# Performance work log

Measured on AMD Instinct MI355X. Metric: run time of the kernel, lower is better.

Reference implementation:

```python
import jax, jax.numpy as jnp
import numpy as np

N = 100000   # nodes
E = 1600000  # edges (avg degree 16)
R = 8        # relations
B = 4        # bases
IN = 128     # in_size
H = 128      # hidden_size
OUT = 64     # out_feats


def setup_inputs() -> dict:
    key = jax.random.key(0)
    k = jax.random.split(key, 14)
    sI = 1.0 / np.sqrt(IN)
    sH = 1.0 / np.sqrt(H)
    sB = 1.0 / np.sqrt(B)
    return {
        "feat": jax.random.normal(k[0], (N, IN), jnp.float32),
        "win": jax.random.normal(k[1], (IN, H), jnp.float32) * sI,
        "bin_": jnp.zeros((H,), jnp.float32),
        "basis0": jax.random.normal(k[2], (B, H, H), jnp.float32) * sH,
        "wcomp0": jax.random.normal(k[3], (R, B), jnp.float32) * sB,
        "loop0": jax.random.normal(k[4], (H, H), jnp.float32) * sH,
        "hbias0": jnp.zeros((H,), jnp.float32),
        "basis1": jax.random.normal(k[5], (B, H, H), jnp.float32) * sH,
        "wcomp1": jax.random.normal(k[6], (R, B), jnp.float32) * sB,
        "loop1": jax.random.normal(k[7], (H, H), jnp.float32) * sH,
        "hbias1": jnp.zeros((H,), jnp.float32),
        "wout": jax.random.normal(k[8], (H, OUT), jnp.float32) * sH,
        "bout": jnp.zeros((OUT,), jnp.float32),
        "src": jax.random.randint(k[9], (E,), 0, N),
        "dst": jax.random.randint(k[10], (E,), 0, N),
        "etypes": jax.random.randint(k[11], (E,), 0, R),
    }


def _rel_graph_conv(h, src, dst, etypes, basis, wcomp, loopw, hbias):
    """DGL RelGraphConv (basis regularizer, self_loop, bias, relu).

    out_i = relu( sum_r W_r * (sum_{e: dst_e=i, etype_e=r} h[src_e]) + h_i @ loopw + bias )
    Messages are linear, so we aggregate raw features by (dst, relation)
    composite key first, then apply the R per-relation matmuls once per node.
    """
    W = jnp.einsum('rb,bio->rio', wcomp, basis)          # [R, H, H] basis-composed weights
    seg = dst * R + etypes                               # composite (node, relation) key
    s = jax.ops.segment_sum(h[src], seg, num_segments=N * R)  # [N*R, H]
    s = s.reshape(N, R, -1)
    agg = jnp.einsum('nri,rio->no', s, W)                # [N, H]
    return jax.nn.relu(agg + hbias + h @ loopw)


def reference(feat, win, bin_, basis0, wcomp0, loop0, hbias0,
              basis1, wcomp1, loop1, hbias1, wout, bout, src, dst, etypes):
    h = jax.nn.relu(feat @ win + bin_)                   # input_layer
    h = _rel_graph_conv(h, src, dst, etypes, basis0, wcomp0, loop0, hbias0)
    h = _rel_graph_conv(h, src, dst, etypes, basis1, wcomp1, loop1, hbias1)
    return jax.nn.relu(h @ wout + bout)                  # out_layer
```

## Files before the change

### kernel.cpp

```cpp
#include <hip/hip_runtime.h>

#define NN   100000
#define EE   1600000
constexpr int RR = 8;
constexpr int BBASES = 4;
constexpr int SCAN_CHUNK = 1024;
constexpr int NBLK = (NN + SCAN_CHUNK - 1) / SCAN_CHUNK;
constexpr int NBUK = 98;
constexpr int EPB  = 4096;
constexpr int P1BLOCKS = (EE + EPB - 1) / EPB;

typedef __attribute__((ext_vector_type(8))) short short8;
typedef __attribute__((ext_vector_type(4))) float f32x4;

__device__ __forceinline__ unsigned pack2(float x, float y) {
    unsigned xu = __float_as_uint(x);
    unsigned yu = __float_as_uint(y);
    xu = (xu + 0x7fffu + ((xu >> 16) & 1u)) >> 16;
    yu = (yu + 0x7fffu + ((yu >> 16) & 1u)) & 0xffff0000u;
    return xu | yu;
}

__device__ __forceinline__ unsigned short bf16r(float x) {
    unsigned u = __float_as_uint(x);
    return (unsigned short)((u + 0x7fffu + ((u >> 16) & 1u)) >> 16);
}

__device__ __forceinline__ void async16(const void* g, void* l) {
    __builtin_amdgcn_global_load_lds(
        (const __attribute__((address_space(1))) void*)g,
        (__attribute__((address_space(3))) void*)l, 16, 0, 0);
}


__global__ __launch_bounds__(256) void count_kernel(const int* __restrict__ dst,
                                                    int* __restrict__ counts) {
    int e = blockIdx.x * 256 + threadIdx.x;
    if (e < EE) atomicAdd(&counts[dst[e]], 1);
}

__global__ __launch_bounds__(256) void scan1(const int* __restrict__ counts,
                                             int* __restrict__ offsets,
                                             int* __restrict__ totals) {
    __shared__ int lds[256];
    int b = blockIdx.x, tid = threadIdx.x;
    int base = b * SCAN_CHUNK + tid * 4;
    int v0 = (base + 0 < NN) ? counts[base + 0] : 0;
    int v1 = (base + 1 < NN) ? counts[base + 1] : 0;
    int v2 = (base + 2 < NN) ? counts[base + 2] : 0;
    int v3 = (base + 3 < NN) ? counts[base + 3] : 0;
    int s0 = v0, s1 = s0 + v1, s2 = s1 + v2, s3 = s2 + v3;
    lds[tid] = s3;
    __syncthreads();
    for (int d = 1; d < 256; d <<= 1) {
        int x = (tid >= d) ? lds[tid - d] : 0;
        __syncthreads();
        lds[tid] += x;
        __syncthreads();
    }
    int incl = lds[tid];
    int prefix = incl - s3;
    if (base + 0 < NN) offsets[base + 0] = prefix;
    if (base + 1 < NN) offsets[base + 1] = prefix + s0;
    if (base + 2 < NN) offsets[base + 2] = prefix + s1;
    if (base + 3 < NN) offsets[base + 3] = prefix + s2;
    if (tid == 255) totals[b] = lds[255];
}

__global__ __launch_bounds__(128) void scan2(int* __restrict__ totals,
                                             int* __restrict__ offsets,
                                             int* __restrict__ gcursor) {
    __shared__ int s[128];
    int tid = threadIdx.x;
    int v = (tid < NBLK) ? totals[tid] : 0;
    s[tid] = v;
    __syncthreads();
    for (int d = 1; d < 128; d <<= 1) {
        int x = (tid >= d) ? s[tid - d] : 0;
        __syncthreads();
        s[tid] += x;
        __syncthreads();
    }
    int excl = s[tid] - v;
    if (tid < NBLK) {
        totals[tid] = excl;
        gcursor[tid] = excl;
    }
    if (tid == NBLK - 1) offsets[NN] = excl + v;
}

__global__ __launch_bounds__(256) void scan3(int* __restrict__ offsets,
                                             const int* __restrict__ totals) {
    int i = blockIdx.x * 256 + threadIdx.x;
    if (i < NN) offsets[i] += totals[i >> 10];
}


__global__ __launch_bounds__(256) void bin_pass1(const int* __restrict__ src,
                                                 const int* __restrict__ dst,
                                                 const int* __restrict__ et,
                                                 int* __restrict__ gcursor,
                                                 unsigned* __restrict__ tmp) {
    __shared__ unsigned stage[EPB];
    __shared__ int hist[128];
    __shared__ int sc[128];
    __shared__ int lb[128];
    __shared__ int gb[128];
    int tid = threadIdx.x;
    long e0 = (long)blockIdx.x * EPB;
    if (tid < 128) hist[tid] = 0;
    __syncthreads();

    unsigned w[16];
    int bk[16], pos[16];
#pragma unroll
    for (int i = 0; i < 16; ++i) {
        long e = e0 + i * 256 + tid;
        bool valid = e < EE;
        int d = valid ? dst[e] : 0;
        int s = valid ? src[e] : 0;
        int r = valid ? et[e] : 0;
        bk[i] = d >> 10;
        w[i] = (unsigned)s | ((unsigned)r << 17) | ((unsigned)(d & 1023) << 20);
        pos[i] = valid ? atomicAdd(&hist[bk[i]], 1) : -1;
    }
    __syncthreads();
    if (tid < 128) sc[tid] = hist[tid];
    __syncthreads();
    for (int d = 1; d < 128; d <<= 1) {
        int v = 0;
        if (tid < 128 && tid >= d) v = sc[tid - d];
        __syncthreads();
        if (tid < 128) sc[tid] += v;
        __syncthreads();
    }
    if (tid < 128) lb[tid] = sc[tid] - hist[tid];
    if (tid < NBUK && hist[tid] > 0) gb[tid] = atomicAdd(&gcursor[tid], hist[tid]);
    __syncthreads();
    int total = sc[127];
#pragma unroll
    for (int i = 0; i < 16; ++i) {
        if (pos[i] >= 0) stage[lb[bk[i]] + pos[i]] = w[i];
    }
    __syncthreads();
    for (int s = tid; s < total; s += 256) {
        int lo = 0, hi = 127;
#pragma unroll
        for (int it = 0; it < 7; ++it) {
            int mid = (lo + hi + 1) >> 1;
            if (lb[mid] <= s) lo = mid; else hi = mid - 1;
        }
        tmp[gb[lo] + (s - lb[lo])] = stage[s];
    }
}

__global__ __launch_bounds__(1024) void bin_pass2(const unsigned* __restrict__ tmp,
                                                  const int* __restrict__ offsets,
                                                  int* __restrict__ packed) {
    __shared__ int hist[8192];
    __shared__ int ssum[1024];
    int b = blockIdx.x, tid = threadIdx.x;
    int nb0 = b << 10;
    int nend = nb0 + 1024; if (nend > NN) nend = NN;
    int beg = offsets[nb0], end = offsets[nend];
#pragma unroll
    for (int i = 0; i < 8; ++i) hist[tid * 8 + i] = 0;
    __syncthreads();
    for (int e = beg + tid; e < end; e += 1024) {
        unsigned wv = tmp[e];
        atomicAdd(&hist[(wv >> 17) & 8191], 1);
    }
    __syncthreads();
    int loc[8];
    int run = 0;
#pragma unroll
    for (int i = 0; i < 8; ++i) { loc[i] = run; run += hist[tid * 8 + i]; }
    ssum[tid] = run;
    __syncthreads();
    for (int d = 1; d < 1024; d <<= 1) {
        int x = (tid >= d) ? ssum[tid - d] : 0;
        __syncthreads();
        ssum[tid] += x;
        __syncthreads();
    }
    int base = (tid > 0) ? ssum[tid - 1] : 0;
#pragma unroll
    for (int i = 0; i < 8; ++i) hist[tid * 8 + i] = base + loc[i];
    __syncthreads();
    for (int e = beg + tid; e < end; e += 1024) {
        unsigned wv = tmp[e];
        int p = beg + atomicAdd(&hist[(wv >> 17) & 8191], 1);
        packed[p] = (int)((wv & 0x1FFFFu) | (((wv >> 17) & 7u) << 20));
    }
}


__global__ __launch_bounds__(256) void convert_weights(const float* __restrict__ basis0,
                                                       const float* __restrict__ loop0,
                                                       const float* __restrict__ basis1,
                                                       const float* __restrict__ loop1,
                                                       const float* __restrict__ win,
                                                       const float* __restrict__ wout,
                                                       unsigned short* __restrict__ BT0,
                                                       unsigned short* __restrict__ BT1,
                                                       unsigned short* __restrict__ winT,
                                                       unsigned short* __restrict__ woutT) {
    int i = blockIdx.x * 256 + threadIdx.x;
    if (i < 81920) {
        int n = i / 640, k = i % 640;
        BT0[i] = bf16r(k < 512 ? basis0[(size_t)k * 128 + n] : loop0[(size_t)(k - 512) * 128 + n]);
    } else if (i < 163840) {
        int j = i - 81920;
        int n = j / 640, k = j % 640;
        BT1[j] = bf16r(k < 512 ? basis1[(size_t)k * 128 + n] : loop1[(size_t)(k - 512) * 128 + n]);
    } else if (i < 180224) {
        int j = i - 163840;
        int n = j >> 7, k = j & 127;
        winT[j] = bf16r(win[(size_t)k * 128 + n]);
    } else if (i < 188416) {
        int j = i - 180224;
        int n = j >> 7, k = j & 127;
        woutT[j] = bf16r(wout[(size_t)k * 64 + n]);
    }
}

template <int NC, bool F32OUT, bool AF32>
__global__ __launch_bounds__(256) void gemm128(const void* __restrict__ Aptr,
                                               const unsigned short* __restrict__ BT,
                                               const float* __restrict__ bias,
                                               void* __restrict__ outp, int M) {
    constexpr int NFRAG = NC / 32;
    constexpr int BQ = NC * 8 / 256;
    __shared__ __align__(16) char As[2][16384];
    __shared__ __align__(16) char Bs[2][NC * 128];
    int tid = threadIdx.x;
    int lane = tid & 63;
    int wave = tid >> 6;
    int wm = wave >> 1, wn = wave & 1;
    int m0 = blockIdx.x * 128;

    uint4 areg[4], breg[BQ];
    auto loadA = [&](int c) {
#pragma unroll
        for (int q = 0; q < 4; ++q) {
            int lin = q * 256 + tid;
            int row = lin >> 3, slot = lin & 7;
            int gr = m0 + row;
            gr = (gr < M) ? gr : (M - 1);
            if (AF32) {
                const float* fp = (const float*)Aptr + (size_t)gr * 128 + c * 64 + slot * 8;
                float4 v0 = *(const float4*)fp;
                float4 v1 = *(const float4*)(fp + 4);
                areg[q].x = pack2(v0.x, v0.y);
                areg[q].y = pack2(v0.z, v0.w);
                areg[q].z = pack2(v1.x, v1.y);
                areg[q].w = pack2(v1.z, v1.w);
            } else {
                areg[q] = *(const uint4*)((const char*)Aptr + (size_t)gr * 256 + c * 128 + slot * 16);
            }
        }
    };
    auto loadB = [&](int c) {
#pragma unroll
        for (int q = 0; q < BQ; ++q) {
            int lin = q * 256 + tid;
            int n = lin >> 3, slot = lin & 7;
            breg[q] = *(const uint4*)((const char*)BT + (size_t)n * 256 + c * 128 + slot * 16);
        }
    };

    f32x4 acc[4][NFRAG];
#pragma unroll
    for (int m = 0; m < 4; ++m)
#pragma unroll
        for (int n = 0; n < NFRAG; ++n) acc[m][n] = (f32x4)0.f;

    loadA(0); loadB(0);
    int swz = (lane & 7) << 4;

    for (int c = 0; c < 2; ++c) {
        int buf = c & 1;
#pragma unroll
        for (int q = 0; q < 4; ++q) {
            int lin = q * 256 + tid;
            int row = lin >> 3, slot = lin & 7;
            *(uint4*)(As[buf] + row * 128 + ((slot * 16) ^ ((row & 7) << 4))) = areg[q];
        }
#pragma unroll
        for (int q = 0; q < BQ; ++q) {
            int lin = q * 256 + tid;
            int row = lin >> 3, slot = lin & 7;
            *(uint4*)(Bs[buf] + row * 128 + ((slot * 16) ^ ((row & 7) << 4))) = breg[q];
        }
        __syncthreads();
        if (c < 1) { loadA(1); loadB(1); }
#pragma unroll
        for (int ks = 0; ks < 2; ++ks) {
            short8 a[4], b[NFRAG];
            int kb = ks * 64 + (lane >> 4) * 16;
#pragma unroll
            for (int m = 0; m < 4; ++m) {
                int row = wm * 64 + m * 16 + (lane & 15);
                a[m] = *(const short8*)(As[buf] + row * 128 + (kb ^ swz));
            }
#pragma unroll
            for (int n = 0; n < NFRAG; ++n) {
                int col = wn * (NC / 2) + n * 16 + (lane & 15);
                b[n] = *(const short8*)(Bs[buf] + col * 128 + (kb ^ swz));
            }
#pragma unroll
            for (int m = 0; m < 4; ++m)
#pragma unroll
                for (int n = 0; n < NFRAG; ++n)
                    acc[m][n] = __builtin_amdgcn_mfma_f32_16x16x32_bf16(a[m], b[n], acc[m][n], 0, 0, 0);
        }
        __syncthreads();
    }

    int colbase = wn * (NC / 2) + (lane & 15);
    float bias_v[NFRAG];
#pragma unroll
    for (int n = 0; n < NFRAG; ++n) bias_v[n] = bias[colbase + n * 16];
#pragma unroll
    for (int m = 0; m < 4; ++m) {
        int rl0 = m0 + wm * 64 + m * 16 + ((lane >> 4) << 2);
#pragma unroll
        for (int n = 0; n < NFRAG; ++n) {
            int col = colbase + n * 16;
#pragma unroll
            for (int q = 0; q < 4; ++q) {
                float v = fmaxf(acc[m][n][q] + bias_v[n], 0.f);
                int row = rl0 + q;
                if (F32OUT) {
                    if (row < M) ((float*)outp)[(size_t)row * NC + col] = v;
                } else {
                    float vo = __shfl_xor(v, 1);
                    if (((lane & 1) == 0) && row < M)
                        ((unsigned*)outp)[(size_t)row * (NC / 2) + (col >> 1)] = pack2(v, vo);
                }
            }
        }
    }
}


__global__ __launch_bounds__(256) void agg_kernel(const unsigned* __restrict__ hin,
                                                  const int* __restrict__ offsets,
                                                  const int* __restrict__ packed,
                                                  const float* __restrict__ wcomp,
                                                  unsigned* __restrict__ tbuf,
                                                  int chunk_start, int chunk_len) {
    __shared__ float wc[32];
    int tid = threadIdx.x;
    if (tid < 32) wc[tid] = wcomp[tid];
    __syncthreads();
    int nl = blockIdx.x * 4 + (tid >> 6);
    int lane = tid & 63;
    if (nl >= chunk_len) return;
    int n = chunk_start + nl;
    int beg = offsets[n], end = offsets[n + 1];

    float t0 = 0.f, t1 = 0.f, t2 = 0.f, t3 = 0.f;
    float t4 = 0.f, t5 = 0.f, t6 = 0.f, t7 = 0.f;
    float sx = 0.f, sy = 0.f;
    int rcur = -1;

    auto fold = [&]() {
        float w0 = wc[rcur * 4 + 0], w1 = wc[rcur * 4 + 1];
        float w2 = wc[rcur * 4 + 2], w3 = wc[rcur * 4 + 3];
        t0 = fmaf(w0, sx, t0); t1 = fmaf(w0, sy, t1);
        t2 = fmaf(w1, sx, t2); t3 = fmaf(w1, sy, t3);
        t4 = fmaf(w2, sx, t4); t5 = fmaf(w2, sy, t5);
        t6 = fmaf(w3, sx, t6); t7 = fmaf(w3, sy, t7);
        sx = 0.f; sy = 0.f;
    };
    auto acc1 = [&](unsigned u, unsigned hv) {
        int r = (int)(u >> 20);
        if (r != rcur) {
            if (rcur >= 0) fold();
            rcur = r;
        }
        sx += __uint_as_float(hv << 16);
        sy += __uint_as_float(hv & 0xffff0000u);
    };

    int e = beg;
    int ehead = (beg + 3) & ~3;
    if (ehead > end) ehead = end;
    for (; e < ehead; ++e) {
        unsigned u = (unsigned)packed[e];
        unsigned hv = hin[(size_t)(u & 0xFFFFFu) * 64 + lane];
        acc1(u, hv);
    }
    for (; e + 8 <= end; e += 8) {
        uint4 p0 = *(const uint4*)(packed + e);
        uint4 p1 = *(const uint4*)(packed + e + 4);
        unsigned h0 = hin[(size_t)(p0.x & 0xFFFFFu) * 64 + lane];
        unsigned h1 = hin[(size_t)(p0.y & 0xFFFFFu) * 64 + lane];
        unsigned h2 = hin[(size_t)(p0.z & 0xFFFFFu) * 64 + lane];
        unsigned h3 = hin[(size_t)(p0.w & 0xFFFFFu) * 64 + lane];
        unsigned h4 = hin[(size_t)(p1.x & 0xFFFFFu) * 64 + lane];
        unsigned h5 = hin[(size_t)(p1.y & 0xFFFFFu) * 64 + lane];
        unsigned h6 = hin[(size_t)(p1.z & 0xFFFFFu) * 64 + lane];
        unsigned h7 = hin[(size_t)(p1.w & 0xFFFFFu) * 64 + lane];
        acc1(p0.x, h0); acc1(p0.y, h1); acc1(p0.z, h2); acc1(p0.w, h3);
        acc1(p1.x, h4); acc1(p1.y, h5); acc1(p1.z, h6); acc1(p1.w, h7);
    }
    for (; e + 4 <= end; e += 4) {
        uint4 p0 = *(const uint4*)(packed + e);
        unsigned h0 = hin[(size_t)(p0.x & 0xFFFFFu) * 64 + lane];
        unsigned h1 = hin[(size_t)(p0.y & 0xFFFFFu) * 64 + lane];
        unsigned h2 = hin[(size_t)(p0.z & 0xFFFFFu) * 64 + lane];
        unsigned h3 = hin[(size_t)(p0.w & 0xFFFFFu) * 64 + lane];
        acc1(p0.x, h0); acc1(p0.y, h1); acc1(p0.z, h2); acc1(p0.w, h3);
    }
    for (; e < end; ++e) {
        unsigned u = (unsigned)packed[e];
        unsigned hv = hin[(size_t)(u & 0xFFFFFu) * 64 + lane];
        acc1(u, hv);
    }
    if (rcur >= 0) fold();

    size_t tb = (size_t)nl * 256 + lane;
    __builtin_nontemporal_store(pack2(t0, t1), &tbuf[tb + 0]);
    __builtin_nontemporal_store(pack2(t2, t3), &tbuf[tb + 64]);
    __builtin_nontemporal_store(pack2(t4, t5), &tbuf[tb + 128]);
    __builtin_nontemporal_store(pack2(t6, t7), &tbuf[tb + 192]);
}


template <bool FUSE_OUT>
__global__ __launch_bounds__(256) void conv_gemm(const unsigned* __restrict__ tbuf,
                                                 const unsigned* __restrict__ hin,
                                                 const unsigned short* __restrict__ BT,
                                                 const float* __restrict__ hbias,
                                                 unsigned* __restrict__ hout,
                                                 const unsigned short* __restrict__ WoutT,
                                                 const float* __restrict__ bout,
                                                 float* __restrict__ outp,
                                                 int chunk_start, int chunk_len) {
    __shared__ __align__(16) char As[2][16384];
    __shared__ __align__(16) char Bs[2][16384];
    __shared__ __align__(16) char Ws[16384];
    int tid = threadIdx.x;
    int lane = tid & 63;
    int wave = tid >> 6;
    int wm = wave >> 1, wn = wave & 1;
    int m0 = blockIdx.x * 128;

    auto stage = [&](int c, int buf) {
#pragma unroll
        for (int q = 0; q < 4; ++q) {
            int row = q * 32 + wave * 8 + (lane >> 3);
            int s_src = (lane & 7) ^ (lane >> 3);
            int lr = m0 + row;
            lr = (lr < chunk_len) ? lr : (chunk_len - 1);
            const char* ga = (c < 8)
                ? (const char*)(tbuf + (size_t)lr * 256) + c * 128 + s_src * 16
                : (const char*)(hin + (size_t)(chunk_start + lr) * 64) + (c - 8) * 128 + s_src * 16;
            async16(ga, &As[buf][q * 4096 + wave * 1024]);
            const char* gb = (const char*)BT + (size_t)row * 1280 + c * 128 + s_src * 16;
            async16(gb, &Bs[buf][q * 4096 + wave * 1024]);
        }
    };

    f32x4 acc[4][4];
#pragma unroll
    for (int m = 0; m < 4; ++m)
#pragma unroll
        for (int n = 0; n < 4; ++n) acc[m][n] = (f32x4)0.f;

    stage(0, 0);
    if (FUSE_OUT) {
#pragma unroll
        for (int q = 0; q < 4; ++q) {
            int row = q * 16 + wave * 4 + (lane >> 4);
            int s_src = (lane & 15) ^ (row & 7);
            async16((const char*)WoutT + (size_t)row * 256 + s_src * 16,
                    &Ws[q * 4096 + wave * 1024]);
        }
    }
    __syncthreads();
    int swz = (lane & 7) << 4;

    for (int c = 0; c < 10; ++c) {
        int buf = c & 1;
        if (c < 9) stage(c + 1, buf ^ 1);
#pragma unroll
        for (int ks = 0; ks < 2; ++ks) {
            short8 a[4], b[4];
            int kb = ks * 64 + (lane >> 4) * 16;
#pragma unroll
            for (int m = 0; m < 4; ++m) {
                int row = wm * 64 + m * 16 + (lane & 15);
                a[m] = *(const short8*)(As[buf] + row * 128 + (kb ^ swz));
            }
#pragma unroll
            for (int n = 0; n < 4; ++n) {
                int col = wn * 64 + n * 16 + (lane & 15);
                b[n] = *(const short8*)(Bs[buf] + col * 128 + (kb ^ swz));
            }
#pragma unroll
            for (int m = 0; m < 4; ++m)
#pragma unroll
                for (int n = 0; n < 4; ++n)
                    acc[m][n] = __builtin_amdgcn_mfma_f32_16x16x32_bf16(a[m], b[n], acc[m][n], 0, 0, 0);
        }
        __syncthreads();
    }

    unsigned* olds = (unsigned*)&As[0][0];
    int colbase = wn * 64 + (lane & 15);
    float bias_v[4];
#pragma unroll
    for (int n = 0; n < 4; ++n) bias_v[n] = hbias[colbase + n * 16];

    if (!FUSE_OUT) {
#pragma unroll
        for (int m = 0; m < 4; ++m) {
            int rbase = wm * 64 + m * 16 + ((lane >> 4) << 2);
#pragma unroll
            for (int n = 0; n < 4; ++n) {
#pragma unroll
                for (int q = 0; q < 4; ++q) {
                    float v = fmaxf(acc[m][n][q] + bias_v[n], 0.f);
                    float vo = __shfl_xor(v, 1);
                    if ((lane & 1) == 0) {
                        olds[(rbase + q) * 64 + wn * 32 + n * 8 + ((lane & 15) >> 1)] = pack2(v, vo);
                    }
                }
            }
        }
        __syncthreads();
#pragma unroll
        for (int i = 0; i < 8; ++i) {
            int j = i * 256 + tid;
            int row = j >> 4, s = j & 15;
            int gr = m0 + row;
            if (gr < chunk_len) {
                ((uint4*)(hout + (size_t)(chunk_start + gr) * 64))[s] = ((const uint4*)olds)[j];
            }
        }
    } else {
#pragma unroll
        for (int m = 0; m < 4; ++m) {
            int rbase = wm * 64 + m * 16 + ((lane >> 4) << 2);
#pragma unroll
            for (int n = 0; n < 4; ++n) {
#pragma unroll
                for (int q = 0; q < 4; ++q) {
                    float v = fmaxf(acc[m][n][q] + bias_v[n], 0.f);
                    float vo = __shfl_xor(v, 1);
                    if ((lane & 1) == 0) {
                        int row = rbase + q;
                        int d = wn * 32 + n * 8 + ((lane & 15) >> 1);
                        olds[row * 64 + (d ^ ((row & 7) << 2))] = pack2(v, vo);
                    }
                }
            }
        }
        __syncthreads();
        f32x4 acc2[4][2];
#pragma unroll
        for (int m = 0; m < 4; ++m)
#pragma unroll
            for (int n = 0; n < 2; ++n) acc2[m][n] = (f32x4)0.f;
#pragma unroll
        for (int ks = 0; ks < 4; ++ks) {
            int kb = ks * 64 + (lane >> 4) * 16;
            short8 a2[4], b2[2];
#pragma unroll
            for (int m = 0; m < 4; ++m) {
                int row = wm * 64 + m * 16 + (lane & 15);
                a2[m] = *(const short8*)((const char*)olds + row * 256 + (kb ^ ((row & 7) << 4)));
            }
#pragma unroll
            for (int n = 0; n < 2; ++n) {
                int col = wn * 32 + n * 16 + (lane & 15);
                b2[n] = *(const short8*)(Ws + col * 256 + (kb ^ ((col & 7) << 4)));
            }
#pragma unroll
            for (int m = 0; m < 4; ++m)
#pragma unroll
                for (int n = 0; n < 2; ++n)
                    acc2[m][n] = __builtin_amdgcn_mfma_f32_16x16x32_bf16(a2[m], b2[n], acc2[m][n], 0, 0, 0);
        }
        int colb = wn * 32 + (lane & 15);
        float bv2[2];
#pragma unroll
        for (int n = 0; n < 2; ++n) bv2[n] = bout[colb + n * 16];
#pragma unroll
        for (int m = 0; m < 4; ++m) {
            int rl0 = wm * 64 + m * 16 + ((lane >> 4) << 2);
#pragma unroll
            for (int n = 0; n < 2; ++n) {
#pragma unroll
                for (int q = 0; q < 4; ++q) {
                    int row = rl0 + q;
                    if (m0 + row < chunk_len) {
                        float v = fmaxf(acc2[m][n][q] + bv2[n], 0.f);
                        outp[(size_t)(chunk_start + m0 + row) * 64 + colb + n * 16] = v;
                    }
                }
            }
        }
    }
}


static inline size_t align256(size_t x) { return (x + 255) & ~(size_t)255; }

extern "C" void kernel_launch(void* const* d_in, const int* in_sizes, int n_in,
                              void* d_out, int out_size, void* d_ws, size_t ws_size,
                              hipStream_t stream) {
    const float* feat   = (const float*)d_in[0];
    const float* win    = (const float*)d_in[1];
    const float* bin_   = (const float*)d_in[2];
    const float* basis0 = (const float*)d_in[3];
    const float* wcomp0 = (const float*)d_in[4];
    const float* loop0  = (const float*)d_in[5];
    const float* hbias0 = (const float*)d_in[6];
    const float* basis1 = (const float*)d_in[7];
    const float* wcomp1 = (const float*)d_in[8];
    const float* loop1  = (const float*)d_in[9];
    const float* hbias1 = (const float*)d_in[10];
    const float* wout   = (const float*)d_in[11];
    const float* bout   = (const float*)d_in[12];
    const int*   src    = (const int*)d_in[13];
    const int*   dst    = (const int*)d_in[14];
    const int*   etyp   = (const int*)d_in[15];
    float* outp = (float*)d_out;

    size_t off = 0;
    char* wsb = (char*)d_ws;
    auto walloc = [&](size_t bytes) { void* p = wsb + off; off += align256(bytes); return p; };
    unsigned* hA  = (unsigned*)walloc((size_t)NN * 64 * 4);
    unsigned* hB  = (unsigned*)walloc((size_t)NN * 64 * 4);
    int* offsets  = (int*)walloc((size_t)(NN + 1) * 4);
    int* counts   = (int*)walloc((size_t)NN * 4);
    int* totals   = (int*)walloc((size_t)NBLK * 4);
    int* gcursor  = (int*)walloc((size_t)NBUK * 4);
    int* packed   = (int*)walloc((size_t)EE * 4);
    unsigned* tmp = (unsigned*)walloc((size_t)EE * 4);
    unsigned short* BT0 = (unsigned short*)walloc((size_t)128 * 640 * 2);
    unsigned short* BT1 = (unsigned short*)walloc((size_t)128 * 640 * 2);
    unsigned short* winT = (unsigned short*)walloc((size_t)128 * 128 * 2);
    unsigned short* woutT = (unsigned short*)walloc((size_t)64 * 128 * 2);
    size_t fixed = off;

    int nchunk = 1;
    while (nchunk < 32) {
        size_t rows = (size_t)(NN + nchunk - 1) / nchunk;
        if (fixed + rows * 1024 <= ws_size) break;
        nchunk *= 2;
    }
    int chunk_rows = (NN + nchunk - 1) / nchunk;
    unsigned* tbuf = (unsigned*)(wsb + fixed);

    hipMemsetAsync(counts, 0, (size_t)NN * 4, stream);
    count_kernel<<<(EE + 255) / 256, 256, 0, stream>>>(dst, counts);
    scan1<<<NBLK, 256, 0, stream>>>(counts, offsets, totals);
    scan2<<<1, 128, 0, stream>>>(totals, offsets, gcursor);
    scan3<<<(NN + 255) / 256, 256, 0, stream>>>(offsets, totals);
    bin_pass1<<<P1BLOCKS, 256, 0, stream>>>(src, dst, etyp, gcursor, tmp);
    bin_pass2<<<NBUK, 1024, 0, stream>>>(tmp, offsets, packed);

    convert_weights<<<(188416 + 255) / 256, 256, 0, stream>>>(
        basis0, loop0, basis1, loop1, win, wout, BT0, BT1, winT, woutT);

    int gblocks = (NN + 127) / 128;
    gemm128<128, false, true><<<gblocks, 256, 0, stream>>>(feat, winT, bin_, hA, NN);

    for (int s = 0; s < NN; s += chunk_rows) {
        int len = (NN - s < chunk_rows) ? (NN - s) : chunk_rows;
        agg_kernel<<<(len + 3) / 4, 256, 0, stream>>>(hA, offsets, packed, wcomp0, tbuf, s, len);
        conv_gemm<false><<<(len + 127) / 128, 256, 0, stream>>>(
            tbuf, hA, BT0, hbias0, hB, nullptr, nullptr, nullptr, s, len);
    }
    for (int s = 0; s < NN; s += chunk_rows) {
        int len = (NN - s < chunk_rows) ? (NN - s) : chunk_rows;
        agg_kernel<<<(len + 3) / 4, 256, 0, stream>>>(hB, offsets, packed, wcomp1, tbuf, s, len);
        conv_gemm<true><<<(len + 127) / 128, 256, 0, stream>>>(
            tbuf, hB, BT1, hbias1, nullptr, woutT, bout, outp, s, len);
    }
}
```

Measured before the change: 424.7 us.

## Aggregate two nodes per wavefront with half-wave 8-byte gathers and masked FMAs

The aggregation kernel now gives each wavefront two destination nodes, one per half-wave. Each lane gathers a uint2 (four bf16 features) per edge instead of one unsigned. The per-relation run-folding is replaced by branch-free direct FMAs into four basis accumulators, with out-of-range edges clamped and masked to zero. The intent is wider gather loads, fewer wavefronts and no divergent fold branches. In exchange it does more FMAs per edge, and the half-wave with the smaller degree idles until the larger one finishes.

Result: faster. 395.0 us (median of 2 runs) (-7.0%).

```diff
diff --git a/kernel.cpp b/kernel.cpp
--- a/kernel.cpp
+++ b/kernel.cpp
@@ -354,78 +354,83 @@
     int tid = threadIdx.x;
     if (tid < 32) wc[tid] = wcomp[tid];
     __syncthreads();
-    int nl = blockIdx.x * 4 + (tid >> 6);
     int lane = tid & 63;
-    if (nl >= chunk_len) return;
-    int n = chunk_start + nl;
-    int beg = offsets[n], end = offsets[n + 1];
-
-    float t0 = 0.f, t1 = 0.f, t2 = 0.f, t3 = 0.f;
-    float t4 = 0.f, t5 = 0.f, t6 = 0.f, t7 = 0.f;
-    float sx = 0.f, sy = 0.f;
-    int rcur = -1;
-
-    auto fold = [&]() {
-        float w0 = wc[rcur * 4 + 0], w1 = wc[rcur * 4 + 1];
-        float w2 = wc[rcur * 4 + 2], w3 = wc[rcur * 4 + 3];
-        t0 = fmaf(w0, sx, t0); t1 = fmaf(w0, sy, t1);
-        t2 = fmaf(w1, sx, t2); t3 = fmaf(w1, sy, t3);
-        t4 = fmaf(w2, sx, t4); t5 = fmaf(w2, sy, t5);
-        t6 = fmaf(w3, sx, t6); t7 = fmaf(w3, sy, t7);
-        sx = 0.f; sy = 0.f;
-    };
-    auto acc1 = [&](unsigned u, unsigned hv) {
-        int r = (int)(u >> 20);
-        if (r != rcur) {
-            if (rcur >= 0) fold();
-            rcur = r;
-        }
-        sx += __uint_as_float(hv << 16);
-        sy += __uint_as_float(hv & 0xffff0000u);
-    };
-
-    int e = beg;
-    int ehead = (beg + 3) & ~3;
-    if (ehead > end) ehead = end;
-    for (; e < ehead; ++e) {
-        unsigned u = (unsigned)packed[e];
-        unsigned hv = hin[(size_t)(u & 0xFFFFFu) * 64 + lane];
-        acc1(u, hv);
-    }
-    for (; e + 8 <= end; e += 8) {
-        uint4 p0 = *(const uint4*)(packed + e);
-        uint4 p1 = *(const uint4*)(packed + e + 4);
-        unsigned h0 = hin[(size_t)(p0.x & 0xFFFFFu) * 64 + lane];
-        unsigned h1 = hin[(size_t)(p0.y & 0xFFFFFu) * 64 + lane];
-        unsigned h2 = hin[(size_t)(p0.z & 0xFFFFFu) * 64 + lane];
-        unsigned h3 = hin[(size_t)(p0.w & 0xFFFFFu) * 64 + lane];
-        unsigned h4 = hin[(size_t)(p1.x & 0xFFFFFu) * 64 + lane];
-        unsigned h5 = hin[(size_t)(p1.y & 0xFFFFFu) * 64 + lane];
-        unsigned h6 = hin[(size_t)(p1.z & 0xFFFFFu) * 64 + lane];
-        unsigned h7 = hin[(size_t)(p1.w & 0xFFFFFu) * 64 + lane];
-        acc1(p0.x, h0); acc1(p0.y, h1); acc1(p0.z, h2); acc1(p0.w, h3);
-        acc1(p1.x, h4); acc1(p1.y, h5); acc1(p1.z, h6); acc1(p1.w, h7);
-    }
-    for (; e + 4 <= end; e += 4) {
-        uint4 p0 = *(const uint4*)(packed + e);
-        unsigned h0 = hin[(size_t)(p0.x & 0xFFFFFu) * 64 + lane];
-        unsigned h1 = hin[(size_t)(p0.y & 0xFFFFFu) * 64 + lane];
-        unsigned h2 = hin[(size_t)(p0.z & 0xFFFFFu) * 64 + lane];
-        unsigned h3 = hin[(size_t)(p0.w & 0xFFFFFu) * 64 + lane];
-        acc1(p0.x, h0); acc1(p0.y, h1); acc1(p0.z, h2); acc1(p0.w, h3);
-    }
-    for (; e < end; ++e) {
-        unsigned u = (unsigned)packed[e];
-        unsigned hv = hin[(size_t)(u & 0xFFFFFu) * 64 + lane];
-        acc1(u, hv);
-    }
-    if (rcur >= 0) fold();
-
-    size_t tb = (size_t)nl * 256 + lane;
-    __builtin_nontemporal_store(pack2(t0, t1), &tbuf[tb + 0]);
-    __builtin_nontemporal_store(pack2(t2, t3), &tbuf[tb + 64]);
-    __builtin_nontemporal_store(pack2(t4, t5), &tbuf[tb + 128]);
-    __builtin_nontemporal_store(pack2(t6, t7), &tbuf[tb + 192]);
+    int half = lane >> 5;
+    int l5 = lane & 31;
+    int pairI = blockIdx.x * 4 + (tid >> 6);
+    int nlA = pairI * 2;
+    if (nlA >= chunk_len) return;
+    bool hasB = (nlA + 1) < chunk_len;
+    int nA = chunk_start + nlA;
+    int begA = offsets[nA];
+    int endA = offsets[nA + 1];
+    int endB = hasB ? offsets[nA + 2] : endA;
+
+    int ebeg = half ? endA : begA;
+    int eend = half ? endB : endA;
+    const uint2* hin2 = (const uint2*)hin;
+
+    float acc[4][4];
+#pragma unroll
+    for (int b = 0; b < 4; ++b)
+#pragma unroll
+        for (int k = 0; k < 4; ++k) acc[b][k] = 0.f;
+
+    int degA = endA - begA;
+    int degB = endB - endA;
+    int steps = (degA > degB) ? degA : degB;
+    int elast = eend - 1; if (elast < 0) elast = 0;
+
+    int e = ebeg;
+    for (int s = 0; s < steps; s += 4) {
+        int i0 = e + 0; i0 = (i0 <= elast) ? i0 : elast;
+        int i1 = e + 1; i1 = (i1 <= elast) ? i1 : elast;
+        int i2 = e + 2; i2 = (i2 <= elast) ? i2 : elast;
+        int i3 = e + 3; i3 = (i3 <= elast) ? i3 : elast;
+        unsigned u0 = (unsigned)packed[i0];
+        unsigned u1 = (unsigned)packed[i1];
+        unsigned u2 = (unsigned)packed[i2];
+        unsigned u3 = (unsigned)packed[i3];
+        uint2 h0 = hin2[(size_t)(u0 & 0xFFFFFu) * 32 + l5];
+        uint2 h1 = hin2[(size_t)(u1 & 0xFFFFFu) * 32 + l5];
+        uint2 h2 = hin2[(size_t)(u2 & 0xFFFFFu) * 32 + l5];
+        uint2 h3 = hin2[(size_t)(u3 & 0xFFFFFu) * 32 + l5];
+#define CONS(u, hv, ei)                                                     \
+        {                                                                   \
+            float m_ = ((ei) < eend) ? 1.f : 0.f;                           \
+            int r_ = (int)((u) >> 20);                                      \
+            float x0_ = __uint_as_float((hv).x << 16) * m_;                 \
+            float y0_ = __uint_as_float((hv).x & 0xffff0000u) * m_;         \
+            float x1_ = __uint_as_float((hv).y << 16) * m_;                 \
+            float y1_ = __uint_as_float((hv).y & 0xffff0000u) * m_;         \
+            _Pragma("unroll")                                               \
+            for (int b = 0; b < 4; ++b) {                                   \
+                float w_ = wc[r_ * 4 + b];                                  \
+                acc[b][0] = fmaf(w_, x0_, acc[b][0]);                       \
+                acc[b][1] = fmaf(w_, y0_, acc[b][1]);                       \
+                acc[b][2] = fmaf(w_, x1_, acc[b][2]);                       \
+                acc[b][3] = fmaf(w_, y1_, acc[b][3]);                       \
+            }                                                               \
+        }
+        CONS(u0, h0, e + 0);
+        CONS(u1, h1, e + 1);
+        CONS(u2, h2, e + 2);
+        CONS(u3, h3, e + 3);
+#undef CONS
+        e += 4;
+    }
+
+    int nlX = nlA + half;
+    if (half == 0 || hasB) {
+        size_t tb = (size_t)nlX * 256 + 2 * l5;
+#pragma unroll
+        for (int b = 0; b < 4; ++b) {
+            uint2 v;
+            v.x = pack2(acc[b][0], acc[b][1]);
+            v.y = pack2(acc[b][2], acc[b][3]);
+            *(uint2*)(tbuf + tb + b * 64) = v;
+        }
+    }
 }
 
 
@@ -640,7 +645,7 @@
     int* counts   = (int*)walloc((size_t)NN * 4);
     int* totals   = (int*)walloc((size_t)NBLK * 4);
     int* gcursor  = (int*)walloc((size_t)NBUK * 4);
-    int* packed   = (int*)walloc((size_t)EE * 4);
+    int* packed   = (int*)walloc((size_t)(EE + 16) * 4);
     unsigned* tmp = (unsigned*)walloc((size_t)EE * 4);
     unsigned short* BT0 = (unsigned short*)walloc((size_t)128 * 640 * 2);
     unsigned short* BT1 = (unsigned short*)walloc((size_t)128 * 640 * 2);
@@ -673,13 +678,15 @@
 
     for (int s = 0; s < NN; s += chunk_rows) {
         int len = (NN - s < chunk_rows) ? (NN - s) : chunk_rows;
-        agg_kernel<<<(len + 3) / 4, 256, 0, stream>>>(hA, offsets, packed, wcomp0, tbuf, s, len);
+        int npairs = (len + 1) / 2;
+        agg_kernel<<<(npairs + 3) / 4, 256, 0, stream>>>(hA, offsets, packed, wcomp0, tbuf, s, len);
         conv_gemm<false><<<(len + 127) / 128, 256, 0, stream>>>(
             tbuf, hA, BT0, hbias0, hB, nullptr, nullptr, nullptr, s, len);
     }
     for (int s = 0; s < NN; s += chunk_rows) {
         int len = (NN - s < chunk_rows) ? (NN - s) : chunk_rows;
-        agg_kernel<<<(len + 3) / 4, 256, 0, stream>>>(hB, offsets, packed, wcomp1, tbuf, s, len);
+        int npairs = (len + 1) / 2;
+        agg_kernel<<<(npairs + 3) / 4, 256, 0, stream>>>(hB, offsets, packed, wcomp1, tbuf, s, len);
         conv_gemm<true><<<(len + 127) / 128, 256, 0, stream>>>(
             tbuf, hB, BT1, hbias1, nullptr, woutT, bout, outp, s, len);
     }
```
